# Optimization experiments

Measured on AMD Instinct MI355X. Metric: run time of the kernel, lower is better.

The kernel has to match this reference:

```python
import jax, jax.numpy as jnp
import numpy as np

# levels for the auction iterations: j = 7..-1 gives level = -4^j, j = -2 gives level = 0
_LEVEL_JS = list(range(7, -3, -1))


def approx_match(xyz1, xyz2):
    # xyz1: [B,N,3], xyz2: [B,M,3] -> soft match matrix [B,N,M]
    B, N, _ = xyz1.shape
    M = xyz2.shape[1]
    multiL = 1.0 if N >= M else float(M // N)
    multiR = float(N // M) if N >= M else 1.0
    # pairwise squared distances [B,N,M]
    d2 = jnp.sum((xyz1[:, :, None, :] - xyz2[:, None, :, :]) ** 2, axis=-1)
    levels = jnp.array([0.0 if j == -2 else -(4.0 ** j) for j in _LEVEL_JS],
                       dtype=xyz1.dtype)

    def step(carry, level):
        match, remainL, remainR = carry
        w = jnp.exp(level * d2) * remainR[:, None, :]                      # [B,N,M]
        # row-normalize to each left point's remaining mass
        w = w * (remainL / (jnp.sum(w, axis=2) + 1e-9))[:, :, None]
        # clip columns to right points' remaining capacity
        ss = jnp.sum(w, axis=1) + 1e-9                                     # [B,M]
        w = w * jnp.minimum(remainR / ss, 1.0)[:, None, :]
        match = match + w
        remainL = jnp.maximum(remainL - jnp.sum(w, axis=2), 0.0)
        remainR = jnp.maximum(remainR - jnp.sum(w, axis=1), 0.0)
        return (match, remainL, remainR), None

    init = (jnp.zeros_like(d2),
            jnp.full((B, N), multiL, dtype=d2.dtype),
            jnp.full((B, M), multiR, dtype=d2.dtype))
    (match, _, _), _ = jax.lax.scan(step, init, levels)
    return match


def match_cost(xyz1, xyz2, match):
    # cost[b] = sum_{k,l} match[b,k,l] * ||xyz1[b,k] - xyz2[b,l]||
    d = jnp.sqrt(jnp.sum((xyz1[:, :, None, :] - xyz2[:, None, :, :]) ** 2, axis=-1))
    return jnp.sum(match * d, axis=(1, 2))


def setup_inputs() -> dict:
    key = jax.random.key(0)
    k1, k2 = jax.random.split(key)
    B, N, M = 8, 2048, 2048
    input1 = jax.random.normal(k1, (B, N, 3), dtype=jnp.float32)
    input2 = jax.random.normal(k2, (B, M, 3), dtype=jnp.float32)
    return {"input1": input1, "input2": input2}


def reference(input1, input2):
    match = approx_match(input1, input2)
    return match_cost(input1, input2, match)
```

## Files before the change

### kernel.cpp

```cpp
#include <hip/hip_runtime.h>
#include <hip/hip_fp16.h>


#define BATCH 8
#define NPTS 2048
#define MPTS 2048
#define BLOCK 256
#define ROWS 16
#define LOG2E 1.44269504088896340736f

__device__ __forceinline__ float fast_exp2(float x) {
  return __builtin_amdgcn_exp2f(x);
}
__device__ __forceinline__ float fast_sqrt(float a) {
  return __builtin_amdgcn_sqrtf(a);
}
__device__ __forceinline__ float packh2(float c, float r) {
  __half2 h = __halves2half2(__float2half_rn(c), __float2half_rn(r));
  return __builtin_bit_cast(float, h);
}

__device__ __forceinline__ void load8(const float4* q, int r0, float k,
                                      float* x, float* y, float* z) {
  int b4 = (r0 >> 2) * 3;
  float4 q0 = q[b4], q1 = q[b4 + 1], q2 = q[b4 + 2];
  float4 q3 = q[b4 + 3], q4 = q[b4 + 4], q5 = q[b4 + 5];
  x[0] = k * q0.x; y[0] = k * q0.y; z[0] = k * q0.z;
  x[1] = k * q0.w; y[1] = k * q1.x; z[1] = k * q1.y;
  x[2] = k * q1.z; y[2] = k * q1.w; z[2] = k * q2.x;
  x[3] = k * q2.y; y[3] = k * q2.z; z[3] = k * q2.w;
  x[4] = k * q3.x; y[4] = k * q3.y; z[4] = k * q3.z;
  x[5] = k * q3.w; y[5] = k * q4.x; z[5] = k * q4.y;
  x[6] = k * q4.z; y[6] = k * q4.w; z[6] = k * q5.x;
  x[7] = k * q5.y; y[7] = k * q5.z; z[7] = k * q5.w;
}

__global__ __launch_bounds__(BLOCK, 4) void emd_A0_kernel(
    const float* __restrict__ xyz1, const float* __restrict__ xyz2,
    float* __restrict__ rowscale, float* __restrict__ out,
    float* __restrict__ t9, float* __restrict__ t1acc,
    float* __restrict__ t1zero, float k0) {
  __shared__ float4 sP[MPTS];
  __shared__ float sRed[ROWS * 4];
  __shared__ float sRs[ROWS];

  const int tid = threadIdx.x;
  const int bid = blockIdx.x;
  const int b = bid >> 7;
  const int t0 = (bid & 127) * ROWS;
  const bool desig = (bid & 127) == 0;
  if (bid == 0 && tid < BATCH) { out[tid] = 0.0f; t9[tid] = 0.0f; }

  const float4* q2 = (const float4*)(xyz2 + (size_t)b * MPTS * 3);
  float4* z4 = (float4*)(t1zero + (size_t)b * MPTS);
  for (int g = tid; g < MPTS / 4; g += BLOCK) {
    float4 a = q2[3 * g], bb = q2[3 * g + 1], c = q2[3 * g + 2];
    sP[4 * g + 0] = make_float4(k0 * a.x, k0 * a.y, k0 * a.z, 0.0f);
    sP[4 * g + 1] = make_float4(k0 * a.w, k0 * bb.x, k0 * bb.y, 0.0f);
    sP[4 * g + 2] = make_float4(k0 * bb.z, k0 * bb.w, k0 * c.x, 0.0f);
    sP[4 * g + 3] = make_float4(k0 * c.y, k0 * c.z, k0 * c.w, 0.0f);
    if (desig) z4[g] = make_float4(0.f, 0.f, 0.f, 0.f);
  }
  __syncthreads();

  const int wave = tid >> 6, lane = tid & 63;
  const int phase = lane >> 1, rg = lane & 1;
  const int r0 = t0 + rg * 8;
  float x1[8], y1[8], z1[8], acc[8];
  load8((const float4*)(xyz1 + (size_t)b * NPTS * 3), r0, k0, x1, y1, z1);
#pragma unroll
  for (int j = 0; j < 8; ++j) acc[j] = 0.0f;
  const int mb = wave * 512 + phase;
#pragma unroll 2
  for (int it = 0; it < 16; ++it) {
    float4 v = sP[mb + it * 32];
#pragma unroll
    for (int j = 0; j < 8; ++j) {
      float dx = x1[j] - v.x, dy = y1[j] - v.y, dz = z1[j] - v.z;
      float s = __builtin_fmaf(dx, dx, __builtin_fmaf(dy, dy, dz * dz));
      acc[j] += fast_exp2(-s);
    }
  }
#pragma unroll
  for (int j = 0; j < 8; ++j) {
    acc[j] += __shfl_xor(acc[j], 2, 64);
    acc[j] += __shfl_xor(acc[j], 4, 64);
    acc[j] += __shfl_xor(acc[j], 8, 64);
    acc[j] += __shfl_xor(acc[j], 16, 64);
    acc[j] += __shfl_xor(acc[j], 32, 64);
  }
  if (lane < 2) {
#pragma unroll
    for (int j = 0; j < 8; ++j) sRed[(rg * 8 + j) * 4 + wave] = acc[j];
  }
  __syncthreads();
  if (tid < ROWS) {
    float s = sRed[tid * 4] + sRed[tid * 4 + 1] + sRed[tid * 4 + 2] +
              sRed[tid * 4 + 3];
    float rs = 1.0f / (s + 1e-9f);
    rowscale[(size_t)b * NPTS + t0 + tid] = rs;
    sRs[tid] = rs;
  }
  __syncthreads();

  float rsn[8];
#pragma unroll
  for (int j = 0; j < 8; ++j) rsn[j] = sRs[rg * 8 + j];
  float* accb = t1acc + (size_t)b * MPTS;
#pragma unroll 2
  for (int it = 0; it < 16; ++it) {
    int idx = mb + it * 32;
    float4 v = sP[idx];
    float part = 0.0f;
#pragma unroll
    for (int j = 0; j < 8; ++j) {
      float dx = x1[j] - v.x, dy = y1[j] - v.y, dz = z1[j] - v.z;
      float s = __builtin_fmaf(dx, dx, __builtin_fmaf(dy, dy, dz * dz));
      part = __builtin_fmaf(fast_exp2(-s), rsn[j], part);
    }
    part += __shfl_xor(part, 1, 64);
    if (rg == 0) atomicAdd(accb + idx, part);
  }
}

template <bool FIRST, bool LAST>
__global__ __launch_bounds__(BLOCK, 4) void emd_CA_kernel(
    const float* __restrict__ xyz1, const float* __restrict__ xyz2,
    float* __restrict__ rowscale, float* __restrict__ remainL,
    const float* __restrict__ rrIn, float* __restrict__ rrOut,
    const float* __restrict__ t1In, float* __restrict__ t1Acc,
    float* __restrict__ t1Zero, float* __restrict__ out,
    float* __restrict__ t9, float kS, float invK) {
  __shared__ float4 sP[MPTS];
  __shared__ float sRedS[ROWS * 4];
  __shared__ float sRedC[ROWS * 4];
  __shared__ float sRedR[ROWS * 4];
  __shared__ float sCost[ROWS];
  __shared__ float sRs[ROWS];

  const int tid = threadIdx.x;
  const int bid = blockIdx.x;
  const int b = bid >> 7;
  const int t0 = (bid & 127) * ROWS;
  const bool desig = (bid & 127) == 0;

  const float4* q2 = (const float4*)(xyz2 + (size_t)b * MPTS * 3);
  const float4* rr4 = (const float4*)(rrIn + (size_t)b * MPTS);
  const float4* t14 = (const float4*)(t1In + (size_t)b * MPTS);
  float4* ro4 = (float4*)(rrOut + (size_t)b * MPTS);
  float4* z4 = LAST ? nullptr : (float4*)(t1Zero + (size_t)b * MPTS);
  for (int g = tid; g < MPTS / 4; g += BLOCK) {
    float4 a = q2[3 * g], bb = q2[3 * g + 1], c = q2[3 * g + 2];
    float4 t1v = t14[g];
    float4 rrv = FIRST ? make_float4(1.f, 1.f, 1.f, 1.f) : rr4[g];
    float cc[4], rn[4];
    float rrc[4] = {rrv.x, rrv.y, rrv.z, rrv.w};
    float t1c[4] = {t1v.x, t1v.y, t1v.z, t1v.w};
#pragma unroll
    for (int i = 0; i < 4; ++i) {
      float colsum = rrc[i] * t1c[i];
      float cs = fminf(rrc[i] / (colsum + 1e-9f), 1.0f);
      cc[i] = rrc[i] * cs;
      rn[i] = fmaxf(rrc[i] - colsum * cs, 0.0f);
    }
    sP[4 * g + 0] = make_float4(kS * a.x, kS * a.y, kS * a.z, packh2(cc[0], rn[0]));
    sP[4 * g + 1] = make_float4(kS * a.w, kS * bb.x, kS * bb.y, packh2(cc[1], rn[1]));
    sP[4 * g + 2] = make_float4(kS * bb.z, kS * bb.w, kS * c.x, packh2(cc[2], rn[2]));
    sP[4 * g + 3] = make_float4(kS * c.y, kS * c.z, kS * c.w, packh2(cc[3], rn[3]));
    if (desig) {
      ro4[g] = make_float4(rn[0], rn[1], rn[2], rn[3]);
      if (!LAST) z4[g] = make_float4(0.f, 0.f, 0.f, 0.f);
    }
  }
  __syncthreads();

  const int wave = tid >> 6, lane = tid & 63;
  const int phase = lane >> 2, rg = lane & 3;
  const int r0 = t0 + rg * 4;
  float x1[4], y1[4], z1[4];
  {
    const float4* q1 = (const float4*)(xyz1 + (size_t)b * NPTS * 3);
    int b4 = (r0 >> 2) * 3;
    float4 a = q1[b4], bb = q1[b4 + 1], c = q1[b4 + 2];
    x1[0] = kS * a.x;  y1[0] = kS * a.y;  z1[0] = kS * a.z;
    x1[1] = kS * a.w;  y1[1] = kS * bb.x; z1[1] = kS * bb.y;
    x1[2] = kS * bb.z; y1[2] = kS * bb.w; z1[2] = kS * c.x;
    x1[3] = kS * c.y;  y1[3] = kS * c.z;  z1[3] = kS * c.w;
  }
  float accS[4] = {0.f, 0.f, 0.f, 0.f};
  float accC[4] = {0.f, 0.f, 0.f, 0.f};
  float accR[4] = {0.f, 0.f, 0.f, 0.f};
  const int mb = wave * 512 + phase;
#pragma unroll 4
  for (int it = 0; it < 32; ++it) {
    float4 v = sP[mb + it * 16];
    __half2 h = __builtin_bit_cast(__half2, v.w);
    float cc = __low2float(h);
    float rr = __high2float(h);
#pragma unroll
    for (int j = 0; j < 4; ++j) {
      float dx = x1[j] - v.x, dy = y1[j] - v.y, dz = z1[j] - v.z;
      float s = __builtin_fmaf(dx, dx, __builtin_fmaf(dy, dy, dz * dz));
      float sq = fast_sqrt(s);
      float e1, e2;
      if (LAST) {
        e2 = 1.0f;
        e1 = fast_exp2(-s);
      } else {
        e2 = fast_exp2(-s);
        float e2s = e2 * e2;
        e1 = e2s * e2s;
      }
      float t = e1 * cc;
      accS[j] += t;
      accC[j] = __builtin_fmaf(t, sq, accC[j]);
      if (LAST) accR[j] += rr;
      else      accR[j] = __builtin_fmaf(e2, rr, accR[j]);
    }
  }
#pragma unroll
  for (int j = 0; j < 4; ++j) {
    accS[j] += __shfl_xor(accS[j], 4, 64);
    accS[j] += __shfl_xor(accS[j], 8, 64);
    accS[j] += __shfl_xor(accS[j], 16, 64);
    accS[j] += __shfl_xor(accS[j], 32, 64);
    accC[j] += __shfl_xor(accC[j], 4, 64);
    accC[j] += __shfl_xor(accC[j], 8, 64);
    accC[j] += __shfl_xor(accC[j], 16, 64);
    accC[j] += __shfl_xor(accC[j], 32, 64);
    accR[j] += __shfl_xor(accR[j], 4, 64);
    accR[j] += __shfl_xor(accR[j], 8, 64);
    accR[j] += __shfl_xor(accR[j], 16, 64);
    accR[j] += __shfl_xor(accR[j], 32, 64);
  }
  if (lane < 4) {
#pragma unroll
    for (int j = 0; j < 4; ++j) {
      sRedS[(rg * 4 + j) * 4 + wave] = accS[j];
      sRedC[(rg * 4 + j) * 4 + wave] = accC[j];
      sRedR[(rg * 4 + j) * 4 + wave] = accR[j];
    }
  }
  __syncthreads();
  if (tid < ROWS) {
    float S2 = sRedS[tid * 4] + sRedS[tid * 4 + 1] + sRedS[tid * 4 + 2] +
               sRedS[tid * 4 + 3];
    float C = sRedC[tid * 4] + sRedC[tid * 4 + 1] + sRedC[tid * 4 + 2] +
              sRedC[tid * 4 + 3];
    float R = sRedR[tid * 4] + sRedR[tid * 4 + 1] + sRedR[tid * 4 + 2] +
              sRedR[tid * 4 + 3];
    size_t idx = (size_t)b * NPTS + t0 + tid;
    float rs = rowscale[idx];
    float rl = FIRST ? 1.0f : remainL[idx];
    float rlN = fmaxf(rl - rs * S2, 0.0f);
    remainL[idx] = rlN;
    float rsN = rlN / (R + 1e-9f);
    rowscale[idx] = rsN;
    sCost[tid] = rs * C * invK;
    sRs[tid] = rsN;
  }
  __syncthreads();
  if (tid == 0) {
    float t = 0.0f;
#pragma unroll
    for (int i = 0; i < ROWS; ++i) t += sCost[i];
    atomicAdd(out + b, t);
    if (LAST) {
      float r = 0.0f;
#pragma unroll
      for (int i = 0; i < ROWS; ++i) r += sRs[i];
      atomicAdd(t9 + b, r);
    }
  }
  if (!LAST) {
    float rsn[4];
#pragma unroll
    for (int j = 0; j < 4; ++j) rsn[j] = sRs[rg * 4 + j];
    float* accb = t1Acc + (size_t)b * MPTS;
#pragma unroll 4
    for (int it = 0; it < 32; ++it) {
      int idx = mb + it * 16;
      float4 v = sP[idx];
      float part = 0.0f;
#pragma unroll
      for (int j = 0; j < 4; ++j) {
        float dx = x1[j] - v.x, dy = y1[j] - v.y, dz = z1[j] - v.z;
        float s = __builtin_fmaf(dx, dx, __builtin_fmaf(dy, dy, dz * dz));
        part = __builtin_fmaf(fast_exp2(-s), rsn[j], part);
      }
      part += __shfl_xor(part, 1, 64);
      part += __shfl_xor(part, 2, 64);
      if (rg == 0) atomicAdd(accb + idx, part);
    }
  }
}

__global__ __launch_bounds__(BLOCK, 4) void emd_C9_kernel(
    const float* __restrict__ xyz1, const float* __restrict__ xyz2,
    const float* __restrict__ rowscale, const float* __restrict__ remainR,
    const float* __restrict__ t9, float* __restrict__ out) {
  __shared__ float4 sP[MPTS];
  __shared__ float sRed[ROWS * 4];
  __shared__ float sCost[ROWS];

  const int tid = threadIdx.x;
  const int bid = blockIdx.x;
  const int b = bid >> 7;
  const int t0 = (bid & 127) * ROWS;
  const int wave = tid >> 6, lane = tid & 63;
  const float t1 = t9[b];

  const float4* q2 = (const float4*)(xyz2 + (size_t)b * MPTS * 3);
  const float4* rr4 = (const float4*)(remainR + (size_t)b * MPTS);
  for (int g = tid; g < MPTS / 4; g += BLOCK) {
    float4 a = q2[3 * g], bb = q2[3 * g + 1], c = q2[3 * g + 2];
    float4 rr = rr4[g];
    float w0 = rr.x * fminf(rr.x / (rr.x * t1 + 1e-9f), 1.0f);
    float w1 = rr.y * fminf(rr.y / (rr.y * t1 + 1e-9f), 1.0f);
    float w2 = rr.z * fminf(rr.z / (rr.z * t1 + 1e-9f), 1.0f);
    float w3 = rr.w * fminf(rr.w / (rr.w * t1 + 1e-9f), 1.0f);
    sP[4 * g + 0] = make_float4(a.x, a.y, a.z, w0);
    sP[4 * g + 1] = make_float4(a.w, bb.x, bb.y, w1);
    sP[4 * g + 2] = make_float4(bb.z, bb.w, c.x, w2);
    sP[4 * g + 3] = make_float4(c.y, c.z, c.w, w3);
  }
  __syncthreads();

  const int phase = lane >> 1, rg = lane & 1;
  const int r0 = t0 + rg * 8;
  float x1[8], y1[8], z1[8], acc[8];
  load8((const float4*)(xyz1 + (size_t)b * NPTS * 3), r0, 1.0f, x1, y1, z1);
#pragma unroll
  for (int j = 0; j < 8; ++j) acc[j] = 0.0f;
  const int mb = wave * 512 + phase;
#pragma unroll 2
  for (int it = 0; it < 16; ++it) {
    float4 v = sP[mb + it * 32];
#pragma unroll
    for (int j = 0; j < 8; ++j) {
      float dx = x1[j] - v.x, dy = y1[j] - v.y, dz = z1[j] - v.z;
      float d2 = __builtin_fmaf(dx, dx, __builtin_fmaf(dy, dy, dz * dz));
      acc[j] = __builtin_fmaf(fast_sqrt(d2), v.w, acc[j]);
    }
  }
#pragma unroll
  for (int j = 0; j < 8; ++j) {
    acc[j] += __shfl_xor(acc[j], 2, 64);
    acc[j] += __shfl_xor(acc[j], 4, 64);
    acc[j] += __shfl_xor(acc[j], 8, 64);
    acc[j] += __shfl_xor(acc[j], 16, 64);
    acc[j] += __shfl_xor(acc[j], 32, 64);
  }
  if (lane < 2) {
#pragma unroll
    for (int j = 0; j < 8; ++j) sRed[(rg * 8 + j) * 4 + wave] = acc[j];
  }
  __syncthreads();
  if (tid < ROWS) {
    float C = sRed[tid * 4] + sRed[tid * 4 + 1] + sRed[tid * 4 + 2] +
              sRed[tid * 4 + 3];
    sCost[tid] = rowscale[(size_t)b * NPTS + t0 + tid] * C;
  }
  __syncthreads();
  if (tid == 0) {
    float t = 0.0f;
#pragma unroll
    for (int i = 0; i < ROWS; ++i) t += sCost[i];
    atomicAdd(out + b, t);
  }
}

extern "C" void kernel_launch(void* const* d_in, const int* in_sizes, int n_in,
                              void* d_out, int out_size, void* d_ws, size_t ws_size,
                              hipStream_t stream) {
  const float* xyz1 = (const float*)d_in[0];
  const float* xyz2 = (const float*)d_in[1];
  float* out = (float*)d_out;
  float* ws = (float*)d_ws;

  const int BN = BATCH * NPTS, BM = BATCH * MPTS;
  float* remainL  = ws;
  float* rowscale = ws + BN;
  float* rrA      = ws + 2 * BN;
  float* rrB      = ws + 2 * BN + BM;
  float* t1b      = ws + 2 * BN + 2 * BM;
  float* t9       = ws + 2 * BN + 5 * BM;

  const float levels[9] = {-16384.f, -4096.f, -1024.f, -256.f, -64.f,
                           -16.f,    -4.f,    -1.f,    -0.25f};
  dim3 grid(BATCH * (NPTS / ROWS));

  hipMemsetAsync(t1b, 0, (size_t)BM * sizeof(float), stream);

  emd_A0_kernel<<<grid, BLOCK, 0, stream>>>(
      xyz1, xyz2, rowscale, out, t9, t1b , t1b + BM ,
      sqrtf(-levels[0] * LOG2E));

  for (int l = 0; l < 9; ++l) {
    float kB = sqrtf(-levels[l] * LOG2E);
    float kA = 0.5f * kB;
    float* cur = t1b + (size_t)(l % 3) * BM;
    float* nxt = t1b + (size_t)((l + 1) % 3) * BM;
    float* zer = t1b + (size_t)((l + 2) % 3) * BM;
    float* rin = (l % 2 == 0) ? rrA : rrB;
    float* rou = (l % 2 == 0) ? rrB : rrA;
    if (l == 0) {
      emd_CA_kernel<true, false><<<grid, BLOCK, 0, stream>>>(
          xyz1, xyz2, rowscale, remainL, rin, rou, cur, nxt, zer, out, t9,
          kA, 1.0f / kA);
    } else if (l < 8) {
      emd_CA_kernel<false, false><<<grid, BLOCK, 0, stream>>>(
          xyz1, xyz2, rowscale, remainL, rin, rou, cur, nxt, zer, out, t9,
          kA, 1.0f / kA);
    } else {
      emd_CA_kernel<false, true><<<grid, BLOCK, 0, stream>>>(
          xyz1, xyz2, rowscale, remainL, rin, rou, cur, nxt, zer, out, t9,
          kB, 1.0f / kB);
    }
  }
  emd_C9_kernel<<<grid, BLOCK, 0, stream>>>(xyz1, xyz2, rowscale, rrB, t9, out);
}
```

Baseline: 357.6 us.

## Fuse all auction iterations into one cooperative persistent kernel with grid syncs

```diff
diff --git a/kernel.cpp b/kernel.cpp
--- a/kernel.cpp
+++ b/kernel.cpp
@@ -1,5 +1,8 @@
 #include <hip/hip_runtime.h>
 #include <hip/hip_fp16.h>
+#include <hip/hip_cooperative_groups.h>
+
+namespace cg = cooperative_groups;
 
 
 #define BATCH 8
@@ -33,6 +36,326 @@
   x[5] = k * q3.w; y[5] = k * q4.x; z[5] = k * q4.y;
   x[6] = k * q4.z; y[6] = k * q4.w; z[6] = k * q5.x;
   x[7] = k * q5.y; y[7] = k * q5.z; z[7] = k * q5.w;
+}
+
+__global__ __launch_bounds__(BLOCK, 4) void emd_fused_kernel(
+    const float* __restrict__ xyz1, const float* __restrict__ xyz2,
+    float* __restrict__ out, float* __restrict__ t1b,
+    float* __restrict__ rrA, float* __restrict__ rrB,
+    float* __restrict__ t9) {
+  cg::grid_group gg = cg::this_grid();
+  __shared__ float4 sP[MPTS];
+  __shared__ float sRedS[ROWS * 4];
+  __shared__ float sRedC[ROWS * 4];
+  __shared__ float sRedR[ROWS * 4];
+  __shared__ float sCost[ROWS];
+  __shared__ float sRowScale[ROWS];
+  __shared__ float sRemainL[ROWS];
+  __shared__ float sRn[4];
+
+  const int tid = threadIdx.x;
+  const int bid = blockIdx.x;
+  const int b = bid >> 7;
+  const int t0 = (bid & 127) * ROWS;
+  const bool desig = (bid & 127) == 0;
+  const int wave = tid >> 6, lane = tid & 63;
+  const size_t bM = (size_t)b * MPTS;
+
+  float* cur = t1b + bM;
+  float* nxt = t1b + (size_t)(BATCH * MPTS) + bM;
+  float* zer = t1b + (size_t)(2 * BATCH * MPTS) + bM;
+  float* rin = rrA + bM;
+  float* rou = rrB + bM;
+
+  const float4* q1 = (const float4*)(xyz1 + (size_t)b * NPTS * 3);
+  const float4* q2 = (const float4*)(xyz2 + bM * 3);
+
+  {
+    float4* z0 = (float4*)cur;
+    float4* z1 = (float4*)nxt;
+    for (int g = tid; g < MPTS / 4; g += BLOCK) {
+      float4 a = q2[3 * g], bb = q2[3 * g + 1], c = q2[3 * g + 2];
+      sP[4 * g + 0] = make_float4(a.x, a.y, a.z, 0.f);
+      sP[4 * g + 1] = make_float4(a.w, bb.x, bb.y, 0.f);
+      sP[4 * g + 2] = make_float4(bb.z, bb.w, c.x, 0.f);
+      sP[4 * g + 3] = make_float4(c.y, c.z, c.w, 0.f);
+      if (desig) {
+        z0[g] = make_float4(0.f, 0.f, 0.f, 0.f);
+        z1[g] = make_float4(0.f, 0.f, 0.f, 0.f);
+      }
+    }
+    if (bid == 0 && tid < BATCH) { out[tid] = 0.f; t9[tid] = 0.f; }
+  }
+  __syncthreads();
+
+  const float nc0 = -16384.0f * LOG2E;
+  {
+    const int ph = lane >> 1, rg = lane & 1;
+    float x1a[8], y1a[8], z1a[8], acc[8];
+    load8(q1, t0 + rg * 8, 1.0f, x1a, y1a, z1a);
+#pragma unroll
+    for (int j = 0; j < 8; ++j) acc[j] = 0.f;
+    const int mb = wave * 512 + ph;
+#pragma unroll 2
+    for (int it = 0; it < 16; ++it) {
+      float4 v = sP[mb + it * 32];
+#pragma unroll
+      for (int j = 0; j < 8; ++j) {
+        float dx = x1a[j] - v.x, dy = y1a[j] - v.y, dz = z1a[j] - v.z;
+        float d2 = __builtin_fmaf(dx, dx, __builtin_fmaf(dy, dy, dz * dz));
+        acc[j] += fast_exp2(nc0 * d2);
+      }
+    }
+#pragma unroll
+    for (int j = 0; j < 8; ++j) {
+      acc[j] += __shfl_xor(acc[j], 2, 64);
+      acc[j] += __shfl_xor(acc[j], 4, 64);
+      acc[j] += __shfl_xor(acc[j], 8, 64);
+      acc[j] += __shfl_xor(acc[j], 16, 64);
+      acc[j] += __shfl_xor(acc[j], 32, 64);
+    }
+    if (lane < 2) {
+#pragma unroll
+      for (int j = 0; j < 8; ++j) sRedS[(rg * 8 + j) * 4 + wave] = acc[j];
+    }
+    __syncthreads();
+    if (tid < ROWS) {
+      float s = sRedS[tid * 4] + sRedS[tid * 4 + 1] + sRedS[tid * 4 + 2] +
+                sRedS[tid * 4 + 3];
+      sRowScale[tid] = 1.0f / (s + 1e-9f);
+    }
+    gg.sync();
+    float rsn[8];
+#pragma unroll
+    for (int j = 0; j < 8; ++j) rsn[j] = sRowScale[rg * 8 + j];
+#pragma unroll 2
+    for (int it = 0; it < 16; ++it) {
+      int idx = mb + it * 32;
+      float4 v = sP[idx];
+      float part = 0.f;
+#pragma unroll
+      for (int j = 0; j < 8; ++j) {
+        float dx = x1a[j] - v.x, dy = y1a[j] - v.y, dz = z1a[j] - v.z;
+        float d2 = __builtin_fmaf(dx, dx, __builtin_fmaf(dy, dy, dz * dz));
+        part = __builtin_fmaf(fast_exp2(nc0 * d2), rsn[j], part);
+      }
+      part += __shfl_xor(part, 1, 64);
+      if (rg == 0) atomicAdd(cur + idx, part);
+    }
+  }
+  gg.sync();
+
+  float x1[4], y1[4], z1[4];
+  {
+    int b4 = ((t0 + (lane & 3) * 4) >> 2) * 3;
+    float4 a = q1[b4], bb = q1[b4 + 1], c = q1[b4 + 2];
+    x1[0] = a.x;  y1[0] = a.y;  z1[0] = a.z;
+    x1[1] = a.w;  y1[1] = bb.x; z1[1] = bb.y;
+    x1[2] = bb.z; y1[2] = bb.w; z1[2] = c.x;
+    x1[3] = c.y;  y1[3] = c.z;  z1[3] = c.w;
+  }
+  const int phc = lane >> 2, rgc = lane & 3;
+  const int mbc = wave * 512 + phc;
+
+  float nc2 = -4096.0f * LOG2E;
+  for (int l = 0; l < 9; ++l) {
+    const bool LAST = (l == 8);
+    float rnsum = 0.f;
+    {
+      const float4* t14 = (const float4*)cur;
+      const float4* rr4 = (const float4*)rin;
+      float4* ro4 = (float4*)rou;
+      float4* z4 = (float4*)zer;
+      for (int g = tid; g < MPTS / 4; g += BLOCK) {
+        float4 t1v = t14[g];
+        float4 rrv = (l == 0) ? make_float4(1.f, 1.f, 1.f, 1.f) : rr4[g];
+        float rrc[4] = {rrv.x, rrv.y, rrv.z, rrv.w};
+        float t1c[4] = {t1v.x, t1v.y, t1v.z, t1v.w};
+        float cc[4], rn[4];
+#pragma unroll
+        for (int i = 0; i < 4; ++i) {
+          float colsum = rrc[i] * t1c[i];
+          float cs = fminf(rrc[i] / (colsum + 1e-9f), 1.0f);
+          cc[i] = rrc[i] * cs;
+          rn[i] = fmaxf(rrc[i] - colsum * cs, 0.f);
+        }
+        rnsum += rn[0] + rn[1] + rn[2] + rn[3];
+        sP[4 * g + 0].w = packh2(cc[0], rn[0]);
+        sP[4 * g + 1].w = packh2(cc[1], rn[1]);
+        sP[4 * g + 2].w = packh2(cc[2], rn[2]);
+        sP[4 * g + 3].w = packh2(cc[3], rn[3]);
+        if (desig) {
+          ro4[g] = make_float4(rn[0], rn[1], rn[2], rn[3]);
+          if (!LAST) z4[g] = make_float4(0.f, 0.f, 0.f, 0.f);
+        }
+      }
+      if (LAST) {
+        rnsum += __shfl_xor(rnsum, 1, 64);
+        rnsum += __shfl_xor(rnsum, 2, 64);
+        rnsum += __shfl_xor(rnsum, 4, 64);
+        rnsum += __shfl_xor(rnsum, 8, 64);
+        rnsum += __shfl_xor(rnsum, 16, 64);
+        rnsum += __shfl_xor(rnsum, 32, 64);
+        if (lane == 0) sRn[wave] = rnsum;
+      }
+    }
+    __syncthreads();
+    float accS[4] = {0.f, 0.f, 0.f, 0.f};
+    float accC[4] = {0.f, 0.f, 0.f, 0.f};
+    float accR[4] = {0.f, 0.f, 0.f, 0.f};
+#pragma unroll 4
+    for (int it = 0; it < 32; ++it) {
+      float4 v = sP[mbc + it * 16];
+      __half2 h = __builtin_bit_cast(__half2, v.w);
+      float cc = __low2float(h);
+      float rr = __high2float(h);
+#pragma unroll
+      for (int j = 0; j < 4; ++j) {
+        float dx = x1[j] - v.x, dy = y1[j] - v.y, dz = z1[j] - v.z;
+        float d2 = __builtin_fmaf(dx, dx, __builtin_fmaf(dy, dy, dz * dz));
+        float sq = fast_sqrt(d2);
+        float e2 = fast_exp2(nc2 * d2);
+        float e2s = e2 * e2;
+        float e1 = e2s * e2s;
+        float t = e1 * cc;
+        accS[j] += t;
+        accC[j] = __builtin_fmaf(t, sq, accC[j]);
+        accR[j] = __builtin_fmaf(e2, rr, accR[j]);
+      }
+    }
+#pragma unroll
+    for (int j = 0; j < 4; ++j) {
+      accS[j] += __shfl_xor(accS[j], 4, 64);
+      accS[j] += __shfl_xor(accS[j], 8, 64);
+      accS[j] += __shfl_xor(accS[j], 16, 64);
+      accS[j] += __shfl_xor(accS[j], 32, 64);
+      accC[j] += __shfl_xor(accC[j], 4, 64);
+      accC[j] += __shfl_xor(accC[j], 8, 64);
+      accC[j] += __shfl_xor(accC[j], 16, 64);
+      accC[j] += __shfl_xor(accC[j], 32, 64);
+      accR[j] += __shfl_xor(accR[j], 4, 64);
+      accR[j] += __shfl_xor(accR[j], 8, 64);
+      accR[j] += __shfl_xor(accR[j], 16, 64);
+      accR[j] += __shfl_xor(accR[j], 32, 64);
+    }
+    if (lane < 4) {
+#pragma unroll
+      for (int j = 0; j < 4; ++j) {
+        sRedS[(rgc * 4 + j) * 4 + wave] = accS[j];
+        sRedC[(rgc * 4 + j) * 4 + wave] = accC[j];
+        sRedR[(rgc * 4 + j) * 4 + wave] = accR[j];
+      }
+    }
+    __syncthreads();
+    if (tid < ROWS) {
+      float S2 = sRedS[tid * 4] + sRedS[tid * 4 + 1] + sRedS[tid * 4 + 2] +
+                 sRedS[tid * 4 + 3];
+      float C = sRedC[tid * 4] + sRedC[tid * 4 + 1] + sRedC[tid * 4 + 2] +
+                sRedC[tid * 4 + 3];
+      float R = sRedR[tid * 4] + sRedR[tid * 4 + 1] + sRedR[tid * 4 + 2] +
+                sRedR[tid * 4 + 3];
+      if (LAST) R = sRn[0] + sRn[1] + sRn[2] + sRn[3];
+      float rs = sRowScale[tid];
+      float rl = (l == 0) ? 1.0f : sRemainL[tid];
+      float rlN = fmaxf(rl - rs * S2, 0.f);
+      sRemainL[tid] = rlN;
+      sRowScale[tid] = rlN / (R + 1e-9f);
+      sCost[tid] = rs * C;
+    }
+    __syncthreads();
+    if (tid == 0) {
+      float t = 0.f;
+#pragma unroll
+      for (int i = 0; i < ROWS; ++i) t += sCost[i];
+      atomicAdd(out + b, t);
+      if (LAST) {
+        float r = 0.f;
+#pragma unroll
+        for (int i = 0; i < ROWS; ++i) r += sRowScale[i];
+        atomicAdd(t9 + b, r);
+      }
+    }
+    if (!LAST) {
+      float rsn[4];
+#pragma unroll
+      for (int j = 0; j < 4; ++j) rsn[j] = sRowScale[rgc * 4 + j];
+#pragma unroll 4
+      for (int it = 0; it < 32; ++it) {
+        int idx = mbc + it * 16;
+        float4 v = sP[idx];
+        float part = 0.f;
+#pragma unroll
+        for (int j = 0; j < 4; ++j) {
+          float dx = x1[j] - v.x, dy = y1[j] - v.y, dz = z1[j] - v.z;
+          float d2 = __builtin_fmaf(dx, dx, __builtin_fmaf(dy, dy, dz * dz));
+          part = __builtin_fmaf(fast_exp2(nc2 * d2), rsn[j], part);
+        }
+        part += __shfl_xor(part, 1, 64);
+        part += __shfl_xor(part, 2, 64);
+        if (rgc == 0) atomicAdd(nxt + idx, part);
+      }
+    }
+    gg.sync();
+    if (!LAST) {
+      float* tp = cur; cur = nxt; nxt = zer; zer = tp;
+      float* tr = rin; rin = rou; rou = tr;
+      nc2 *= 0.25f;
+    }
+  }
+
+  {
+    const float t1 = t9[b];
+    const float4* rr4 = (const float4*)rou;
+    for (int g = tid; g < MPTS / 4; g += BLOCK) {
+      float4 rr = rr4[g];
+      sP[4 * g + 0].w = rr.x * fminf(rr.x / (__builtin_fmaf(rr.x, t1, 1e-9f)), 1.0f);
+      sP[4 * g + 1].w = rr.y * fminf(rr.y / (__builtin_fmaf(rr.y, t1, 1e-9f)), 1.0f);
+      sP[4 * g + 2].w = rr.z * fminf(rr.z / (__builtin_fmaf(rr.z, t1, 1e-9f)), 1.0f);
+      sP[4 * g + 3].w = rr.w * fminf(rr.w / (__builtin_fmaf(rr.w, t1, 1e-9f)), 1.0f);
+    }
+    __syncthreads();
+    const int ph = lane >> 1, rg = lane & 1;
+    float x1a[8], y1a[8], z1a[8], acc[8];
+    load8(q1, t0 + rg * 8, 1.0f, x1a, y1a, z1a);
+#pragma unroll
+    for (int j = 0; j < 8; ++j) acc[j] = 0.f;
+    const int mb = wave * 512 + ph;
+#pragma unroll 2
+    for (int it = 0; it < 16; ++it) {
+      float4 v = sP[mb + it * 32];
+#pragma unroll
+      for (int j = 0; j < 8; ++j) {
+        float dx = x1a[j] - v.x, dy = y1a[j] - v.y, dz = z1a[j] - v.z;
+        float d2 = __builtin_fmaf(dx, dx, __builtin_fmaf(dy, dy, dz * dz));
+        acc[j] = __builtin_fmaf(fast_sqrt(d2), v.w, acc[j]);
+      }
+    }
+#pragma unroll
+    for (int j = 0; j < 8; ++j) {
+      acc[j] += __shfl_xor(acc[j], 2, 64);
+      acc[j] += __shfl_xor(acc[j], 4, 64);
+      acc[j] += __shfl_xor(acc[j], 8, 64);
+      acc[j] += __shfl_xor(acc[j], 16, 64);
+      acc[j] += __shfl_xor(acc[j], 32, 64);
+    }
+    if (lane < 2) {
+#pragma unroll
+      for (int j = 0; j < 8; ++j) sRedS[(rg * 8 + j) * 4 + wave] = acc[j];
+    }
+    __syncthreads();
+    if (tid < ROWS) {
+      float C = sRedS[tid * 4] + sRedS[tid * 4 + 1] + sRedS[tid * 4 + 2] +
+                sRedS[tid * 4 + 3];
+      sCost[tid] = sRowScale[tid] * C;
+    }
+    __syncthreads();
+    if (tid == 0) {
+      float t = 0.f;
+#pragma unroll
+      for (int i = 0; i < ROWS; ++i) t += sCost[i];
+      atomicAdd(out + b, t);
+    }
+  }
 }
 
 __global__ __launch_bounds__(BLOCK, 4) void emd_A0_kernel(
@@ -370,14 +693,8 @@
   }
 }
 
-extern "C" void kernel_launch(void* const* d_in, const int* in_sizes, int n_in,
-                              void* d_out, int out_size, void* d_ws, size_t ws_size,
-                              hipStream_t stream) {
-  const float* xyz1 = (const float*)d_in[0];
-  const float* xyz2 = (const float*)d_in[1];
-  float* out = (float*)d_out;
-  float* ws = (float*)d_ws;
-
+static void launch_fallback(const float* xyz1, const float* xyz2, float* out,
+                            float* ws, hipStream_t stream) {
   const int BN = BATCH * NPTS, BM = BATCH * MPTS;
   float* remainL  = ws;
   float* rowscale = ws + BN;
@@ -391,11 +708,9 @@
   dim3 grid(BATCH * (NPTS / ROWS));
 
   hipMemsetAsync(t1b, 0, (size_t)BM * sizeof(float), stream);
-
   emd_A0_kernel<<<grid, BLOCK, 0, stream>>>(
-      xyz1, xyz2, rowscale, out, t9, t1b , t1b + BM ,
+      xyz1, xyz2, rowscale, out, t9, t1b, t1b + BM,
       sqrtf(-levels[0] * LOG2E));
-
   for (int l = 0; l < 9; ++l) {
     float kB = sqrtf(-levels[l] * LOG2E);
     float kA = 0.5f * kB;
@@ -420,3 +735,41 @@
   }
   emd_C9_kernel<<<grid, BLOCK, 0, stream>>>(xyz1, xyz2, rowscale, rrB, t9, out);
 }
+
+extern "C" void kernel_launch(void* const* d_in, const int* in_sizes, int n_in,
+                              void* d_out, int out_size, void* d_ws, size_t ws_size,
+                              hipStream_t stream) {
+  const float* xyz1 = (const float*)d_in[0];
+  const float* xyz2 = (const float*)d_in[1];
+  float* out = (float*)d_out;
+  float* ws = (float*)d_ws;
+
+  static int mode = -1;
+  if (mode < 0) {
+    int dev = 0;
+    hipGetDevice(&dev);
+    hipDeviceProp_t prop;
+    int maxb = 0;
+    hipError_t e1 = hipGetDeviceProperties(&prop, dev);
+    hipError_t e2 = hipOccupancyMaxActiveBlocksPerMultiprocessor(
+        &maxb, (const void*)emd_fused_kernel, BLOCK, 0);
+    mode = (e1 == hipSuccess && e2 == hipSuccess && prop.cooperativeLaunch &&
+            maxb * prop.multiProcessorCount >= BATCH * (NPTS / ROWS)) ? 1 : 0;
+  }
+
+  if (mode == 1) {
+    const int BM = BATCH * MPTS;
+    float* rrA = ws;
+    float* rrB = ws + BM;
+    float* t1b = ws + 2 * BM;
+    float* t9  = ws + 5 * BM;
+    void* args[] = {(void*)&xyz1, (void*)&xyz2, (void*)&out, (void*)&t1b,
+                    (void*)&rrA, (void*)&rrB, (void*)&t9};
+    hipError_t err = hipLaunchCooperativeKernel(
+        (const void*)emd_fused_kernel, dim3(BATCH * (NPTS / ROWS)),
+        dim3(BLOCK), args, 0, stream);
+    if (err == hipSuccess) return;
+    mode = 0;
+  }
+  launch_fallback(xyz1, xyz2, out, ws, stream);
+}
```

Result: no change. 358.7 us (+0.3%).
